# Performance work log

Measured on AMD Instinct MI355X. Metric: run time of the kernel, lower is better.

Reference implementation:

```python
import jax, jax.numpy as jnp
import numpy as np

N, E = 50000, 800000
IN_FEATS, H, F = 128, 2, 64
NEG_SLOPE = 0.2


def _gat_conv(x, W, attn_l, attn_r, bias, src, dst):
    """DGL-style GATConv. x:[N,IN], W:[H*F,IN], attn_l/attn_r:[H,F], bias:[H*F]. Returns [N,H,F]."""
    z = (x @ W.T).reshape(N, H, F)                      # node projections
    el = jnp.einsum('nhf,hf->nh', z, attn_l)            # [N,H]
    er = jnp.einsum('nhf,hf->nh', z, attn_r)            # [N,H]
    e = jax.nn.leaky_relu(el[src] + er[dst], NEG_SLOPE) # [E,H] edge logits
    # edge softmax over incoming edges of each destination node
    m = jax.ops.segment_max(e, dst, num_segments=N)     # [N,H]
    ex = jnp.exp(e - m[dst])
    s = jax.ops.segment_sum(ex, dst, num_segments=N)    # [N,H]
    alpha = ex / s[dst]                                 # [E,H]
    msg = alpha[:, :, None] * z[src]                    # [E,H,F]
    out = jax.ops.segment_sum(msg, dst, num_segments=N) # [N,H,F]
    return out + bias.reshape(1, H, F)


def setup_inputs() -> dict:
    key = jax.random.key(0)
    ks = jax.random.split(key, 10)
    x = jax.random.normal(ks[0], (N, IN_FEATS), dtype=jnp.float32)
    h = jax.random.normal(ks[1], (N, H, F), dtype=jnp.float32)
    src = jax.random.randint(ks[2], (E,), 0, N, dtype=jnp.int32)
    dst = jax.random.randint(ks[3], (E,), 0, N, dtype=jnp.int32)
    sc = 1.0 / np.sqrt(IN_FEATS)
    W = jax.random.normal(ks[4], (3, H * F, IN_FEATS), dtype=jnp.float32) * sc  # r,u,c fc weights
    attn_l = jax.random.normal(ks[5], (3, H, F), dtype=jnp.float32) * 0.1
    attn_r = jax.random.normal(ks[6], (3, H, F), dtype=jnp.float32) * 0.1
    conv_bias = jax.random.normal(ks[7], (3, H * F), dtype=jnp.float32) * 0.02
    gate_bias = jax.random.uniform(ks[8], (3, H, F), dtype=jnp.float32)  # torch.rand init
    return {"x": x, "h": h, "W": W, "attn_l": attn_l, "attn_r": attn_r,
            "conv_bias": conv_bias, "gate_bias": gate_bias, "src": src, "dst": dst}


def reference(x, h, W, attn_l, attn_r, conv_bias, gate_bias, src, dst):
    # r, u, c gates; each GATConv is applied to x (use_hidden=False branch)
    r = jax.nn.sigmoid(_gat_conv(x, W[0], attn_l[0], attn_r[0], conv_bias[0], src, dst) + gate_bias[0])
    u = jax.nn.sigmoid(_gat_conv(x, W[1], attn_l[1], attn_r[1], conv_bias[1], src, dst) + gate_bias[1])
    # note: original computes h_ = r*h but never uses it in this branch (dead code)
    c = jax.nn.sigmoid(_gat_conv(x, W[2], attn_l[2], attn_r[2], conv_bias[2], src, dst) + gate_bias[2])
    new_h = u * h + (1.0 - u) * c
    return new_h
```

## Files before the change

### kernel.cpp

```cpp
#include <hip/hip_runtime.h>
#include <hip/hip_bf16.h>
#include <math.h>

#define NN 50000
#define EE 800000
#define KIN 128
#define HFD 128
#define ZC 256
#define NB 196
#define GB 782
#define SB 782
#define CAP 64

typedef __bf16 bf16_t;
typedef __bf16 bf16x4 __attribute__((ext_vector_type(4)));
typedef __bf16 bf16x8 __attribute__((ext_vector_type(8)));
typedef float f32x4 __attribute__((ext_vector_type(4)));

__device__ __forceinline__ float ldf(const void* p, size_t i, int isf32) {
    return isf32 ? ((const float*)p)[i] : (float)((const bf16_t*)p)[i];
}
__device__ __forceinline__ bf16x8 load8bf(const void* base, size_t off, int isf32) {
    if (isf32) {
        const float4* p = (const float4*)((const float*)base + off);
        float4 u = p[0], v = p[1];
        bf16x8 r;
        r[0] = (bf16_t)u.x; r[1] = (bf16_t)u.y; r[2] = (bf16_t)u.z; r[3] = (bf16_t)u.w;
        r[4] = (bf16_t)v.x; r[5] = (bf16_t)v.y; r[6] = (bf16_t)v.z; r[7] = (bf16_t)v.w;
        return r;
    }
    return *(const bf16x8*)((const bf16_t*)base + off);
}

__global__ __launch_bounds__(256) void k_front(const unsigned short* __restrict__ xw,
                                               const void* __restrict__ W,
                                               const void* __restrict__ attn_l,
                                               const void* __restrict__ attn_r,
                                               int* __restrict__ deg,
                                               int* __restrict__ dflag,
                                               bf16_t* __restrict__ walv)
{
    const int b = blockIdx.x, tid = threadIdx.x;
    int i = b * 256 + tid;
    if (i < NN) deg[i] = 0;
    if (b > 8) return;

    __shared__ int cnt;
    if (tid == 0) cnt = 0;
    __syncthreads();
    int c = 0;
    for (int k = tid; k < 2048; k += 256) {
        int e = (xw[k] >> 7) & 0xFF;
        if (e > 150) c++;
    }
    atomicAdd(&cnt, c);
    __syncthreads();
    const int isf32 = (cnt > 20) ? 1 : 0;

    if (b == 0) {
        if (tid == 0) dflag[0] = isf32;
        return;
    }
    const int c8 = b - 1;
    const int side = c8 >> 2, g = (c8 >> 1) & 1, h = c8 & 1;
    const void* attn = side ? attn_r : attn_l;
    const int k = tid;
    if (k < KIN) {
        float acc = 0.f;
        for (int f = 0; f < 64; f++) {
            float wv = ldf(W, ((size_t)(g + 1) * HFD + h * 64 + f) * KIN + k, isf32);
            float av = ldf(attn, (size_t)((g + 1) * 2 + h) * 64 + f, isf32);
            acc += wv * av;
        }
        walv[(size_t)c8 * KIN + k] = (bf16_t)acc;
    }
}

__global__ __launch_bounds__(256) void k_big(const void* __restrict__ x,
                                             const void* __restrict__ W,
                                             const bf16_t* __restrict__ walv,
                                             bf16_t* __restrict__ z,
                                             float* __restrict__ eln,
                                             float* __restrict__ ern,
                                             const int* __restrict__ src,
                                             const int* __restrict__ dst,
                                             int* __restrict__ deg,
                                             int* __restrict__ ssrc,
                                             const int* __restrict__ dflag)
{
    __shared__ bf16_t wlds[256 * 128];

    if (blockIdx.x >= GB) {
        int base = (blockIdx.x - GB) * 1024 + threadIdx.x * 4;
        if (base < EE) {
            int4 s4 = *(const int4*)(src + base);
            int4 d4 = *(const int4*)(dst + base);
            int p0 = atomicAdd(&deg[d4.x], 1);
            int p1 = atomicAdd(&deg[d4.y], 1);
            int p2 = atomicAdd(&deg[d4.z], 1);
            int p3 = atomicAdd(&deg[d4.w], 1);
            if (p0 < CAP) ssrc[d4.x * CAP + p0] = s4.x;
            if (p1 < CAP) ssrc[d4.y * CAP + p1] = s4.y;
            if (p2 < CAP) ssrc[d4.z * CAP + p2] = s4.z;
            if (p3 < CAP) ssrc[d4.w * CAP + p3] = s4.w;
        }
        return;
    }

    const int isf32 = dflag[0];
    const int tid = threadIdx.x;

    for (int c = tid; c < 4096; c += 256) {
        int col = c >> 4, g8 = c & 15;
        int g = col >> 7, wc = col & 127;
        bf16x8 v = load8bf(W, ((size_t)(g + 1) * HFD + wc) * KIN + g8 * 8, isf32);
        *(bf16x8*)(wlds + (size_t)col * 128 + (g8 ^ (col & 15)) * 8) = v;
    }

    const int wave = tid >> 6;
    const int lane = tid & 63;
    const int quad = lane >> 4;
    const int lm   = lane & 15;
    const int node_base = blockIdx.x * 64 + wave * 16;

    int nld = node_base + lm;
    if (nld > NN - 1) nld = NN - 1;

    bf16x8 a[4];
#pragma unroll
    for (int kk = 0; kk < 4; kk++)
        a[kk] = load8bf(x, (size_t)nld * KIN + kk * 32 + quad * 8, isf32);

    __syncthreads();

#pragma unroll 4
    for (int t = 0; t < 16; t++) {
        const int col = t * 16 + lm;
        f32x4 acc = {0.f, 0.f, 0.f, 0.f};
#pragma unroll
        for (int kk = 0; kk < 4; kk++) {
            bf16x8 b = *(const bf16x8*)(wlds + (size_t)col * 128 + ((kk * 4 + quad) ^ lm) * 8);
            acc = __builtin_amdgcn_mfma_f32_16x16x32_bf16(a[kk], b, acc, 0, 0, 0);
        }
#pragma unroll
        for (int r = 0; r < 4; r++) {
            int nn = node_base + quad * 4 + r;
            if (nn < NN)
                z[(size_t)nn * ZC + col] = (bf16_t)acc[r];
        }
    }

    {
        f32x4 acc = {0.f, 0.f, 0.f, 0.f};
#pragma unroll
        for (int kk = 0; kk < 4; kk++) {
            bf16x8 b;
            if (lm < 8) b = *(const bf16x8*)(walv + (size_t)lm * KIN + kk * 32 + quad * 8);
            else {
#pragma unroll
                for (int j = 0; j < 8; j++) b[j] = (bf16_t)0.f;
            }
            acc = __builtin_amdgcn_mfma_f32_16x16x32_bf16(a[kk], b, acc, 0, 0, 0);
        }
#pragma unroll
        for (int r = 0; r < 4; r++) {
            int nn = node_base + quad * 4 + r;
            if (nn < NN) {
                if (lm < 4)      eln[(size_t)nn * 4 + lm] = acc[r];
                else if (lm < 8) ern[(size_t)nn * 4 + (lm - 4)] = acc[r];
            }
        }
    }
}

__global__ __launch_bounds__(256) void k_agg(const bf16_t* __restrict__ z,
                                             const int* __restrict__ deg,
                                             const int* __restrict__ ssrc,
                                             const float* __restrict__ eln,
                                             const float* __restrict__ ern,
                                             const void* __restrict__ conv_bias,
                                             const void* __restrict__ gate_bias,
                                             const void* __restrict__ hin,
                                             void* __restrict__ out,
                                             const int* __restrict__ dflag)
{
    const int isf32 = dflag[0];
    const int wave = threadIdx.x >> 6;
    const int lane = threadIdx.x & 63;
    const int j = lane >> 4;
    const int n = blockIdx.x * 4 + wave;
    if (n >= NN) return;
    int cnt = deg[n];
    if (cnt > CAP) cnt = CAP;
    const int* row = ssrc + (size_t)n * CAP;
    const float erj = ern[(size_t)n * 4 + j];
    const size_t zoff = 4 * lane;

    float a0 = 0.f, a1 = 0.f, a2 = 0.f, a3 = 0.f;
    float s = 0.f;
    int i = 0;
    for (; i + 8 <= cnt; i += 8) {
        int sn[8];
#pragma unroll
        for (int q = 0; q < 8; q++) sn[q] = row[i + q];
        bf16x4 p[8];
#pragma unroll
        for (int q = 0; q < 8; q++)
            p[q] = *(const bf16x4*)(z + (size_t)sn[q] * ZC + zoff);
        float w[8];
#pragma unroll
        for (int q = 0; q < 8; q++) {
            float v = eln[(size_t)sn[q] * 4 + j] + erj;
            v = v > 0.f ? v : 0.2f * v;
            w[q] = __expf(v);
        }
#pragma unroll
        for (int q = 0; q < 8; q++) {
            a0 += w[q] * (float)p[q][0];
            a1 += w[q] * (float)p[q][1];
            a2 += w[q] * (float)p[q][2];
            a3 += w[q] * (float)p[q][3];
            s += w[q];
        }
    }
    if (i + 4 <= cnt) {
        int sn[4];
#pragma unroll
        for (int q = 0; q < 4; q++) sn[q] = row[i + q];
        bf16x4 p[4];
#pragma unroll
        for (int q = 0; q < 4; q++)
            p[q] = *(const bf16x4*)(z + (size_t)sn[q] * ZC + zoff);
#pragma unroll
        for (int q = 0; q < 4; q++) {
            float v = eln[(size_t)sn[q] * 4 + j] + erj;
            v = v > 0.f ? v : 0.2f * v;
            float w = __expf(v);
            a0 += w * (float)p[q][0];
            a1 += w * (float)p[q][1];
            a2 += w * (float)p[q][2];
            a3 += w * (float)p[q][3];
            s += w;
        }
        i += 4;
    }
    for (; i < cnt; i++) {
        int sn = row[i];
        float v = eln[(size_t)sn * 4 + j] + erj;
        bf16x4 p = *(const bf16x4*)(z + (size_t)sn * ZC + zoff);
        v = v > 0.f ? v : 0.2f * v;
        float w = __expf(v);
        a0 += w * (float)p[0];
        a1 += w * (float)p[1];
        a2 += w * (float)p[2];
        a3 += w * (float)p[3];
        s += w;
    }

    float inv = (cnt > 0) ? 1.f / fmaxf(s, 1e-30f) : 0.f;
    float o[4] = {a0 * inv, a1 * inv, a2 * inv, a3 * inv};

    float res[4];
    float hh[4];
    if (lane < 32) {
#pragma unroll
        for (int t = 0; t < 4; t++)
            hh[t] = ldf(hin, (size_t)n * HFD + 4 * lane + t, isf32);
    }
#pragma unroll
    for (int t = 0; t < 4; t++) {
        int c = 4 * lane + t;
        int gate = c >> 7;
        int cf = c & 127;
        int h = cf >> 6, f = cf & 63;
        float ob = ldf(conv_bias, (size_t)(gate + 1) * 128 + cf, isf32)
                 + ldf(gate_bias, (size_t)((gate + 1) * 2 + h) * 64 + f, isf32);
        float gv = 1.f / (1.f + __expf(-(o[t] + ob)));
        float other = __shfl(gv, lane ^ 32, 64);
        if (lane < 32)
            res[t] = gv * hh[t] + (1.f - gv) * other;
    }
    if (lane < 32) {
        if (isf32) {
            float4 v = {res[0], res[1], res[2], res[3]};
            *(float4*)((float*)out + (size_t)n * HFD + 4 * lane) = v;
        } else {
            bf16x4 v;
            v[0] = (bf16_t)res[0]; v[1] = (bf16_t)res[1];
            v[2] = (bf16_t)res[2]; v[3] = (bf16_t)res[3];
            *(bf16x4*)((bf16_t*)out + (size_t)n * HFD + 4 * lane) = v;
        }
    }
}

extern "C" void kernel_launch(void* const* d_in, const int* in_sizes, int n_in,
                              void* d_out, int out_size, void* d_ws, size_t ws_size,
                              hipStream_t stream)
{
    const void* x         = d_in[0];
    const void* hin       = d_in[1];
    const void* W         = d_in[2];
    const void* attn_l    = d_in[3];
    const void* attn_r    = d_in[4];
    const void* conv_bias = d_in[5];
    const void* gate_bias = d_in[6];
    const int* src        = (const int*)d_in[7];
    const int* dst        = (const int*)d_in[8];

    char* p = (char*)d_ws;
    int* dflag    = (int*)p;    p += 256;
    bf16_t* z     = (bf16_t*)p; p += (size_t)NN * ZC * 2;
    float* eln    = (float*)p;  p += (size_t)NN * 4 * 4;
    float* ern    = (float*)p;  p += (size_t)NN * 4 * 4;
    int* deg      = (int*)p;    p += (size_t)NN * 4;
    int* ssrc     = (int*)p;    p += (size_t)NN * CAP * 4;
    bf16_t* walv  = (bf16_t*)p; p += 8 * KIN * 2;

    k_front<<<NB, 256, 0, stream>>>((const unsigned short*)x, W, attn_l, attn_r,
                                    deg, dflag, walv);
    k_big<<<GB + SB, 256, 0, stream>>>(x, W, walv, z, eln, ern, src, dst,
                                       deg, ssrc, dflag);
    k_agg<<<(NN + 3) / 4, 256, 0, stream>>>(z, deg, ssrc, eln, ern,
                                            conv_bias, gate_bias, hin, d_out, dflag);
}
```

Before: 253.9 us.

## Split projection GEMM across two blocks per node tile and stage z stores through LDS

The projection kernel now gives each 64-node tile two blocks, one per gate group (u and c), so each block loads half the weight matrix into LDS (32 KB instead of 64 KB). That doubles the number of GEMM blocks and can raise occupancy. Results are held in registers, transposed through padded LDS, and written as 16-byte vectors per node row instead of scattered 2-byte stores. The attention-logit MFMA runs only in the g==0 block. In exchange, the x tile is loaded twice and two extra block barriers are added.

```diff
diff --git a/kernel.cpp b/kernel.cpp
--- a/kernel.cpp
+++ b/kernel.cpp
@@ -8,9 +8,10 @@
 #define HFD 128
 #define ZC 256
 #define NB 196
-#define GB 782
+#define GB2 1564
 #define SB 782
 #define CAP 64
+#define TRS 132
 
 typedef __bf16 bf16_t;
 typedef __bf16 bf16x4 __attribute__((ext_vector_type(4)));
@@ -88,10 +89,10 @@
                                              int* __restrict__ ssrc,
                                              const int* __restrict__ dflag)
 {
-    __shared__ bf16_t wlds[256 * 128];
-
-    if (blockIdx.x >= GB) {
-        int base = (blockIdx.x - GB) * 1024 + threadIdx.x * 4;
+    __shared__ bf16_t wlds[128 * 128];
+
+    if (blockIdx.x >= GB2) {
+        int base = (blockIdx.x - GB2) * 1024 + threadIdx.x * 4;
         if (base < EE) {
             int4 s4 = *(const int4*)(src + base);
             int4 d4 = *(const int4*)(dst + base);
@@ -109,11 +110,12 @@
 
     const int isf32 = dflag[0];
     const int tid = threadIdx.x;
-
-    for (int c = tid; c < 4096; c += 256) {
+    const int ng = blockIdx.x >> 1;
+    const int g  = blockIdx.x & 1;
+
+    for (int c = tid; c < 2048; c += 256) {
         int col = c >> 4, g8 = c & 15;
-        int g = col >> 7, wc = col & 127;
-        bf16x8 v = load8bf(W, ((size_t)(g + 1) * HFD + wc) * KIN + g8 * 8, isf32);
+        bf16x8 v = load8bf(W, ((size_t)(g + 1) * HFD + col) * KIN + g8 * 8, isf32);
         *(bf16x8*)(wlds + (size_t)col * 128 + (g8 ^ (col & 15)) * 8) = v;
     }
 
@@ -121,7 +123,7 @@
     const int lane = tid & 63;
     const int quad = lane >> 4;
     const int lm   = lane & 15;
-    const int node_base = blockIdx.x * 64 + wave * 16;
+    const int node_base = ng * 64 + wave * 16;
 
     int nld = node_base + lm;
     if (nld > NN - 1) nld = NN - 1;
@@ -133,25 +135,21 @@
 
     __syncthreads();
 
-#pragma unroll 4
-    for (int t = 0; t < 16; t++) {
-        const int col = t * 16 + lm;
-        f32x4 acc = {0.f, 0.f, 0.f, 0.f};
+    f32x4 acc[8];
+#pragma unroll
+    for (int t = 0; t < 8; t++) {
+        const int wc = t * 16 + lm;
+        f32x4 a4 = {0.f, 0.f, 0.f, 0.f};
 #pragma unroll
         for (int kk = 0; kk < 4; kk++) {
-            bf16x8 b = *(const bf16x8*)(wlds + (size_t)col * 128 + ((kk * 4 + quad) ^ lm) * 8);
-            acc = __builtin_amdgcn_mfma_f32_16x16x32_bf16(a[kk], b, acc, 0, 0, 0);
-        }
-#pragma unroll
-        for (int r = 0; r < 4; r++) {
-            int nn = node_base + quad * 4 + r;
-            if (nn < NN)
-                z[(size_t)nn * ZC + col] = (bf16_t)acc[r];
-        }
-    }
-
-    {
-        f32x4 acc = {0.f, 0.f, 0.f, 0.f};
+            bf16x8 b = *(const bf16x8*)(wlds + (size_t)wc * 128 + ((kk * 4 + quad) ^ lm) * 8);
+            a4 = __builtin_amdgcn_mfma_f32_16x16x32_bf16(a[kk], b, a4, 0, 0, 0);
+        }
+        acc[t] = a4;
+    }
+
+    if (g == 0) {
+        f32x4 sacc = {0.f, 0.f, 0.f, 0.f};
 #pragma unroll
         for (int kk = 0; kk < 4; kk++) {
             bf16x8 b;
@@ -160,16 +158,34 @@
 #pragma unroll
                 for (int j = 0; j < 8; j++) b[j] = (bf16_t)0.f;
             }
-            acc = __builtin_amdgcn_mfma_f32_16x16x32_bf16(a[kk], b, acc, 0, 0, 0);
+            sacc = __builtin_amdgcn_mfma_f32_16x16x32_bf16(a[kk], b, sacc, 0, 0, 0);
         }
 #pragma unroll
         for (int r = 0; r < 4; r++) {
             int nn = node_base + quad * 4 + r;
             if (nn < NN) {
-                if (lm < 4)      eln[(size_t)nn * 4 + lm] = acc[r];
-                else if (lm < 8) ern[(size_t)nn * 4 + (lm - 4)] = acc[r];
+                if (lm < 4)      eln[(size_t)nn * 4 + lm] = sacc[r];
+                else if (lm < 8) ern[(size_t)nn * 4 + (lm - 4)] = sacc[r];
             }
         }
+    }
+
+    __syncthreads();
+#pragma unroll
+    for (int t = 0; t < 8; t++) {
+#pragma unroll
+        for (int r = 0; r < 4; r++)
+            wlds[(size_t)(wave * 16 + quad * 4 + r) * TRS + t * 16 + lm] = (bf16_t)acc[t][r];
+    }
+    __syncthreads();
+#pragma unroll
+    for (int q = 0; q < 4; q++) {
+        int node64 = q * 16 + (tid >> 4);
+        int chunk  = tid & 15;
+        bf16x8 v = *(const bf16x8*)(wlds + (size_t)node64 * TRS + chunk * 8);
+        int node = ng * 64 + node64;
+        if (node < NN)
+            *(bf16x8*)(z + (size_t)node * ZC + g * 128 + chunk * 8) = v;
     }
 }
 
@@ -318,8 +334,8 @@
 
     k_front<<<NB, 256, 0, stream>>>((const unsigned short*)x, W, attn_l, attn_r,
                                     deg, dflag, walv);
-    k_big<<<GB + SB, 256, 0, stream>>>(x, W, walv, z, eln, ern, src, dst,
-                                       deg, ssrc, dflag);
+    k_big<<<GB2 + SB, 256, 0, stream>>>(x, W, walv, z, eln, ern, src, dst,
+                                        deg, ssrc, dflag);
     k_agg<<<(NN + 3) / 4, 256, 0, stream>>>(z, deg, ssrc, eln, ern,
                                             conv_bias, gate_bias, hin, d_out, dflag);
 }
```

Result: no change. 253.7 us (-0.1%).
